# Kernel tuning notes

Hardware: AMD Instinct MI355X
Metric: run time of the kernel (lower is better)

Reference implementation:

```python
import jax, jax.numpy as jnp
import numpy as np

EMBED_DIM = 512
KERNEL = 17


def setup_inputs() -> dict:
    key = jax.random.key(0)
    ks = jax.random.split(key, 5)
    B, L, C = 2, 8192, EMBED_DIM
    s = C ** -0.5
    x = jax.random.normal(ks[0], (B, L, C), dtype=jnp.float32)
    # weights stored as (in, out); equivalent to torch Linear weight.T
    w_qkv = jax.random.normal(ks[1], (C, 3 * C), dtype=jnp.float32) * s
    w_width = jax.random.normal(ks[2], (C, 1), dtype=jnp.float32) * s
    b_width = jax.random.normal(ks[3], (1,), dtype=jnp.float32) * 0.01
    w_out = jax.random.normal(ks[4], (C, C), dtype=jnp.float32) * s
    return {"x": x, "w_qkv": w_qkv, "w_width": w_width, "b_width": b_width, "w_out": w_out}


def reference(x, w_qkv, w_width, b_width, w_out):
    B, L, C = x.shape
    K = KERNEL
    half_k = K // 2
    scale = C ** -0.5

    qkv = x @ w_qkv                      # [B,L,3C]
    q, k, v = jnp.split(qkv, 3, axis=-1)

    # learned soft window width in [1, K]
    width = jax.nn.sigmoid(x @ w_width + b_width) * (K - 1) + 1.0   # [B,L,1]

    # sliding windows of k/v: pad along L then gather K-sized windows
    k_pad = jnp.pad(k, ((0, 0), (half_k, half_k), (0, 0)))
    v_pad = jnp.pad(v, ((0, 0), (half_k, half_k), (0, 0)))
    idx = jnp.arange(L)[:, None] + jnp.arange(K)[None, :]           # [L,K]
    k_win = k_pad[:, idx]                # [B,L,K,C]
    v_win = v_pad[:, idx]                # [B,L,K,C]

    scores = jnp.einsum('blc,blkc->blk', q, k_win) * scale          # [B,L,K]

    rel_pos = jnp.abs(jnp.arange(K, dtype=jnp.float32) - half_k)    # [K]
    soft_mask = jax.nn.sigmoid((width - rel_pos) * 5.0)             # [B,L,K]
    scores = scores - (1.0 - soft_mask) * 10000.0

    attn = jax.nn.softmax(scores, axis=-1)
    out = jnp.einsum('blk,blkc->blc', attn, v_win)                  # [B,L,C]
    return (out + v) @ w_out
```

## Files before the change

kernel.cpp:

```cpp
#include <hip/hip_runtime.h>

typedef unsigned short u16;
typedef unsigned int   u32;
typedef __attribute__((ext_vector_type(8))) short          shortx8;
typedef __attribute__((ext_vector_type(8))) unsigned short ushortx8;
typedef __attribute__((ext_vector_type(4))) float          floatx4;

#define AS1 __attribute__((address_space(1)))
#define AS3 __attribute__((address_space(3)))

#define SEG 8208
#define LV  16416

__device__ __forceinline__ float b2f(u16 v) {
  return __uint_as_float(((u32)v) << 16);
}
__device__ __forceinline__ u16 f2b(float f) {
  u32 u = __float_as_uint(f);
  u += 0x7FFF + ((u >> 16) & 1);
  return (u16)(u >> 16);
}
__device__ __forceinline__ void cp16(const void* g, void* l) {
  __builtin_amdgcn_global_load_lds((AS1 u32*)g, (AS3 u32*)l, 16, 0, 0);
}

__global__ __launch_bounds__(256)
void prep(const float* __restrict__ x, const float* __restrict__ w_width,
          const float* __restrict__ b_width, const float* __restrict__ w_qkv,
          const float* __restrict__ w_out, u16* __restrict__ xb,
          float* __restrict__ width, u16* __restrict__ wqkvT,
          u16* __restrict__ woutT, u16* __restrict__ Vt) {
  __shared__ u16 tile[32][33];
  const int b = blockIdx.x;
  if (b < 4096) {
    const int lane = threadIdx.x & 63;
    const int row  = b * 4 + (threadIdx.x >> 6);
    const float* xp = x + (size_t)row * 512 + lane * 8;
    floatx4 v0 = *(const floatx4*)xp;
    floatx4 v1 = *(const floatx4*)(xp + 4);
    floatx4 w0 = *(const floatx4*)(w_width + lane * 8);
    floatx4 w1 = *(const floatx4*)(w_width + lane * 8 + 4);
    float s = 0.f;
    ushortx8 o;
#pragma unroll
    for (int j = 0; j < 4; ++j) {
      s += v0[j] * w0[j] + v1[j] * w1[j];
      o[j] = f2b(v0[j]); o[4 + j] = f2b(v1[j]);
    }
    *(ushortx8*)(xb + (size_t)row * 512 + lane * 8) = o;
#pragma unroll
    for (int m = 32; m >= 1; m >>= 1) s += __shfl_xor(s, m, 64);
    if (lane == 0)
      width[row] = 16.f / (1.f + __expf(-(s + b_width[0]))) + 1.f;
  } else if (b < 5120) {
    const float* in; u16* out; int R, C, t;
    if (b < 4864) { in = w_qkv; out = wqkvT; R = 512; C = 1536; t = b - 4096; }
    else          { in = w_out; out = woutT; R = 512; C = 512;  t = b - 4864; }
    const int nbx = C / 32;
    const int cb = (t % nbx) * 32;
    const int rb = (t / nbx) * 32;
    const int tx = threadIdx.x & 31;
    const int ty = threadIdx.x >> 5;
#pragma unroll
    for (int i = 0; i < 32; i += 8)
      tile[ty + i][tx] = f2b(in[(size_t)(rb + ty + i) * C + cb + tx]);
    __syncthreads();
#pragma unroll
    for (int i = 0; i < 32; i += 8)
      out[(size_t)(cb + ty + i) * R + rb + tx] = tile[tx][ty + i];
  } else {
    const int idx = (b - 5120) * 256 + threadIdx.x;
    const int ch = idx >> 5;
    const int k  = idx & 31;
    const int seg = k >> 4;
    const int j   = k & 15;
    const int col = seg * SEG + (j < 8 ? j : 8192 + j);
    Vt[(size_t)ch * LV + col] = 0;
  }
}

template <int MODE>
__global__ __launch_bounds__(256, 3)
void gemm_bt(const u16* __restrict__ A, const u16* __restrict__ Bt,
             void* __restrict__ C0, u16* __restrict__ Kb, u16* __restrict__ Vt) {
  const int K = 512;
  __shared__ alignas(16) u16 lds[17408];
  u16* As = lds;
  u16* Bs = lds + 8192;
  const int tid  = threadIdx.x;
  const int lane = tid & 63;
  const int wave = tid >> 6;
  const int quad = lane >> 4;
  const int lr   = lane & 15;
  const int row0 = blockIdx.x * 128;
  const int col0 = blockIdx.y * 128;
  const int wr   = (wave >> 1) * 64;
  const int wc   = (wave & 1) * 64;

  floatx4 acc[4][4];
#pragma unroll
  for (int i = 0; i < 4; ++i)
#pragma unroll
    for (int j = 0; j < 4; ++j) acc[i][j] = (floatx4)0.0f;

  int srow[4], scol[4];
#pragma unroll
  for (int p = 0; p < 4; ++p) {
    int c = p * 256 + tid;
    srow[p] = c >> 3;
    scol[p] = ((c & 7) ^ (srow[p] & 7)) * 8;
  }
  const int swz = lr & 7;

  for (int k0 = 0; k0 < K; k0 += 64) {
#pragma unroll
    for (int p = 0; p < 4; ++p)
      cp16(A + (size_t)(row0 + srow[p]) * K + k0 + scol[p], &As[(p * 256 + tid) * 8]);
#pragma unroll
    for (int p = 0; p < 4; ++p)
      cp16(Bt + (size_t)(col0 + srow[p]) * K + k0 + scol[p], &Bs[(p * 256 + tid) * 8]);
    __syncthreads();

#pragma unroll
    for (int ks = 0; ks < 2; ++ks) {
      shortx8 af[4], bf[4];
#pragma unroll
      for (int mi = 0; mi < 4; ++mi)
        af[mi] = *(const shortx8*)
            &As[((wr + mi * 16 + lr) * 8 + ((ks * 4 + quad) ^ swz)) * 8];
#pragma unroll
      for (int ni = 0; ni < 4; ++ni)
        bf[ni] = *(const shortx8*)
            &Bs[((wc + ni * 16 + lr) * 8 + ((ks * 4 + quad) ^ swz)) * 8];
#pragma unroll
      for (int mi = 0; mi < 4; ++mi)
#pragma unroll
        for (int ni = 0; ni < 4; ++ni)
          acc[mi][ni] = __builtin_amdgcn_mfma_f32_16x16x32_bf16(
              af[mi], bf[ni], acc[mi][ni], 0, 0, 0);
    }
    __syncthreads();
  }

  if constexpr (MODE == 1) {
    if (col0 < 1024) {
      u16* dst = (col0 < 512) ? (u16*)C0 : Kb;
      const int cb = col0 & 511;
#pragma unroll
      for (int mi = 0; mi < 4; ++mi)
#pragma unroll
        for (int ni = 0; ni < 4; ++ni)
#pragma unroll
          for (int r = 0; r < 4; ++r)
            lds[(wr + mi * 16 + quad * 4 + r) * 136 + wc + ni * 16 + lr] =
                f2b(acc[mi][ni][r]);
      __syncthreads();
      const int rr = tid >> 4, cc = (tid & 15) * 8;
#pragma unroll
      for (int it = 0; it < 8; ++it) {
        int row = it * 16 + rr;
        *(ushortx8*)(dst + (size_t)(row0 + row) * 512 + cb + cc) =
            *(const ushortx8*)&lds[row * 136 + cc];
      }
    } else {
      const int cb = col0 - 1024;
      const int bb = row0 >> 13, pib0 = row0 & 8191;
#pragma unroll
      for (int mi = 0; mi < 4; ++mi)
#pragma unroll
        for (int ni = 0; ni < 4; ++ni)
#pragma unroll
          for (int r = 0; r < 4; ++r)
            lds[(wc + ni * 16 + lr) * 136 + wr + mi * 16 + quad * 4 + r] =
                f2b(acc[mi][ni][r]);
      __syncthreads();
      const int rr = tid >> 4, cc = (tid & 15) * 8;
#pragma unroll
      for (int it = 0; it < 8; ++it) {
        int chl = it * 16 + rr;
        ushortx8 v = *(const ushortx8*)&lds[chl * 136 + cc];
        *(ushortx8*)(Vt + (size_t)(cb + chl) * LV + (size_t)bb * SEG + 8 + pib0 + cc) = v;
      }
    }
  } else {
    float* Cf = (float*)C0;
#pragma unroll
    for (int mi = 0; mi < 4; ++mi)
#pragma unroll
      for (int ni = 0; ni < 4; ++ni)
#pragma unroll
        for (int r = 0; r < 4; ++r) {
          int row = row0 + wr + mi * 16 + quad * 4 + r;
          int col = col0 + wc + ni * 16 + lr;
          Cf[(size_t)row * 512 + col] = acc[mi][ni][r];
        }
  }
}

__global__ __launch_bounds__(256)
void attn_mfma(const u16* __restrict__ Q, const u16* __restrict__ Kb,
               const u16* __restrict__ Vt, const float* __restrict__ width,
               u16* __restrict__ Out) {
  __shared__ float Sp[8][16][16];
  __shared__ u16   P[16][32];
  __shared__ u16   O[4][16][136];
  const int tid  = threadIdx.x;
  const int lane = tid & 63;
  const int wave = tid >> 6;
  const int quad = lane >> 4;
  const int lr   = lane & 15;
  const int p0   = blockIdx.x * 16;
  const int pib0 = p0 & 8191;
  const int bb   = p0 >> 13;

  floatx4 s0 = (floatx4)0.0f, s1 = (floatx4)0.0f;
#pragma unroll
  for (int s = 0; s < 4; ++s) {
    const int k0 = wave * 128 + s * 32 + quad * 8;
    shortx8 af = *(const shortx8*)(Q  + (size_t)(p0 + lr) * 512 + k0);
    shortx8 f0 = *(const shortx8*)(Kb + (ptrdiff_t)(p0 - 8 + lr) * 512 + k0);
    shortx8 f1 = *(const shortx8*)(Kb + (ptrdiff_t)(p0 + 8 + lr) * 512 + k0);
    s0 = __builtin_amdgcn_mfma_f32_16x16x32_bf16(af, f0, s0, 0, 0, 0);
    s1 = __builtin_amdgcn_mfma_f32_16x16x32_bf16(af, f1, s1, 0, 0, 0);
  }
#pragma unroll
  for (int r = 0; r < 4; ++r) {
    Sp[wave * 2 + 0][quad * 4 + r][lr] = s0[r];
    Sp[wave * 2 + 1][quad * 4 + r][lr] = s1[r];
  }
  __syncthreads();

  {
    const int row = tid >> 4, cg = tid & 15;
    const float scale = 0.044194173824159216f;
    const float wrow  = width[p0 + row];
    float sv[2]; float mx = -1e30f;
#pragma unroll
    for (int t = 0; t < 2; ++t) {
      const int col = t * 16 + cg;
      float s = Sp[t][row][cg] + Sp[2 + t][row][cg] +
                Sp[4 + t][row][cg] + Sp[6 + t][row][cg];
      const int d  = col - row;
      const int jb = pib0 + col - 8;
      const bool inband  = (d >= 0) && (d <= 16);
      const bool inbatch = ((unsigned)jb < 8192u);
      float rel  = fabsf((float)(d - 8));
      float mask = 1.f / (1.f + __expf(-5.f * (wrow - rel)));
      float pen  = (1.f - mask) * 10000.f;
      float val  = inband ? ((inbatch ? s * scale : 0.f) - pen) : -1e30f;
      sv[t] = val;
      mx = fmaxf(mx, val);
    }
#pragma unroll
    for (int m = 8; m >= 1; m >>= 1) mx = fmaxf(mx, __shfl_xor(mx, m, 64));
    float e0 = __expf(sv[0] - mx), e1 = __expf(sv[1] - mx);
    float sum = e0 + e1;
#pragma unroll
    for (int m = 8; m >= 1; m >>= 1) sum += __shfl_xor(sum, m, 64);
    const float inv = 1.f / sum;
    P[row][cg]      = f2b(e0 * inv + ((cg - row) == 8 ? 1.f : 0.f));
    P[row][cg + 16] = f2b(e1 * inv + ((cg + 16 - row) == 8 ? 1.f : 0.f));
  }
  __syncthreads();

  shortx8 pf = *(const shortx8*)&P[lr][quad * 8];
  const size_t cb0 = (size_t)bb * SEG + pib0;
#pragma unroll
  for (int ct = 0; ct < 8; ++ct) {
    const int ch = wave * 128 + ct * 16 + lr;
    shortx8 vf = *(const shortx8*)(Vt + (size_t)ch * LV + cb0 + quad * 8);
    floatx4 o = __builtin_amdgcn_mfma_f32_16x16x32_bf16(pf, vf, (floatx4)0.0f,
                                                        0, 0, 0);
#pragma unroll
    for (int r = 0; r < 4; ++r)
      O[wave][quad * 4 + r][ct * 16 + lr] = f2b(o[r]);
  }
  __syncthreads();
  {
    const int orow = lane >> 2;
#pragma unroll
    for (int i = 0; i < 4; ++i) {
      const int c = i * 32 + (lane & 3) * 8;
      ushortx8 v = *(const ushortx8*)&O[wave][orow][c];
      *(ushortx8*)(Out + (size_t)(p0 + orow) * 512 + wave * 128 + c) = v;
    }
  }
}

extern "C" void kernel_launch(void* const* d_in, const int* in_sizes, int n_in,
                              void* d_out, int out_size, void* d_ws, size_t ws_size,
                              hipStream_t stream) {
  const float* x       = (const float*)d_in[0];
  const float* w_qkv   = (const float*)d_in[1];
  const float* w_width = (const float*)d_in[2];
  const float* b_width = (const float*)d_in[3];
  const float* w_out   = (const float*)d_in[4];
  float* out = (float*)d_out;

  const int M = 16384, C = 512, N3 = 1536;
  char* ws = (char*)d_ws;
  u16*   xb    = (u16*)(ws);
  u16*   Qb    = (u16*)(ws + 16777216);
  u16*   Kb    = (u16*)(ws + 33554432 + 8192);
  u16*   Vt    = (u16*)(ws + 50348032);
  u16*   wqkvT = (u16*)(ws + 67158016);
  u16*   woutT = (u16*)(ws + 68730880);
  float* width = (float*)(ws + 69255168);

  dim3 blk(256);
  prep<<<dim3(5184), blk, 0, stream>>>(x, w_width, b_width, w_qkv, w_out,
                                       xb, width, wqkvT, woutT, Vt);
  gemm_bt<1><<<dim3(M / 128, N3 / 128), blk, 0, stream>>>(xb, wqkvT, Qb, Kb, Vt);
  attn_mfma<<<dim3(M / 16), blk, 0, stream>>>(Qb, Kb, Vt, width, Qb);
  gemm_bt<2><<<dim3(M / 128, C / 128), blk, 0, stream>>>(Qb, woutT, out, nullptr, nullptr);
}
```

Before: 156.9 us.

## Fuse sliding-window attention with output projection GEMM in one kernel

Merges the attention kernel and the final output-projection GEMM into a single kernel. Each block now handles 64 rows, with one wave per 16 rows computing the full 512-channel score reduction itself, so the LDS partial-sum exchange and its syncs go away. The bf16 attention output (plus v) is staged in a swizzled LDS tile and multiplied directly by woutT, which avoids writing the intermediate to global memory and a separate launch. In exchange, each block rereads woutT from global/L2, there are only 256 blocks with launch_bounds(256,1), and each thread holds large accumulator arrays, which may hurt occupancy and latency hiding.

```diff
diff --git a/kernel.cpp b/kernel.cpp
--- a/kernel.cpp
+++ b/kernel.cpp
@@ -197,94 +197,124 @@
   }
 }
 
-__global__ __launch_bounds__(256)
-void attn_mfma(const u16* __restrict__ Q, const u16* __restrict__ Kb,
-               const u16* __restrict__ Vt, const float* __restrict__ width,
-               u16* __restrict__ Out) {
-  __shared__ float Sp[8][16][16];
-  __shared__ u16   P[16][32];
-  __shared__ u16   O[4][16][136];
+__global__ __launch_bounds__(256, 1)
+void attn_fused(const u16* __restrict__ Q, const u16* __restrict__ Kb,
+                const u16* __restrict__ Vt, const float* __restrict__ width,
+                const u16* __restrict__ woutT, float* __restrict__ Out) {
+  __shared__ alignas(16) u16 Osw[64 * 256];
+  __shared__ alignas(16) u16 P[4][16][32];
   const int tid  = threadIdx.x;
   const int lane = tid & 63;
   const int wave = tid >> 6;
   const int quad = lane >> 4;
   const int lr   = lane & 15;
-  const int p0   = blockIdx.x * 16;
-  const int pib0 = p0 & 8191;
-  const int bb   = p0 >> 13;
+  const int p0   = blockIdx.x * 64;
+  const int pw   = p0 + wave * 16;
+  const int pibw = pw & 8191;
+  const int bb   = pw >> 13;
 
   floatx4 s0 = (floatx4)0.0f, s1 = (floatx4)0.0f;
-#pragma unroll
-  for (int s = 0; s < 4; ++s) {
-    const int k0 = wave * 128 + s * 32 + quad * 8;
-    shortx8 af = *(const shortx8*)(Q  + (size_t)(p0 + lr) * 512 + k0);
-    shortx8 f0 = *(const shortx8*)(Kb + (ptrdiff_t)(p0 - 8 + lr) * 512 + k0);
-    shortx8 f1 = *(const shortx8*)(Kb + (ptrdiff_t)(p0 + 8 + lr) * 512 + k0);
+#pragma unroll 4
+  for (int s = 0; s < 16; ++s) {
+    const int k0 = s * 32 + quad * 8;
+    shortx8 af = *(const shortx8*)(Q  + (size_t)(pw + lr) * 512 + k0);
+    shortx8 f0 = *(const shortx8*)(Kb + (ptrdiff_t)(pw - 8 + lr) * 512 + k0);
+    shortx8 f1 = *(const shortx8*)(Kb + (ptrdiff_t)(pw + 8 + lr) * 512 + k0);
     s0 = __builtin_amdgcn_mfma_f32_16x16x32_bf16(af, f0, s0, 0, 0, 0);
     s1 = __builtin_amdgcn_mfma_f32_16x16x32_bf16(af, f1, s1, 0, 0, 0);
   }
-#pragma unroll
-  for (int r = 0; r < 4; ++r) {
-    Sp[wave * 2 + 0][quad * 4 + r][lr] = s0[r];
-    Sp[wave * 2 + 1][quad * 4 + r][lr] = s1[r];
-  }
-  __syncthreads();
 
   {
-    const int row = tid >> 4, cg = tid & 15;
     const float scale = 0.044194173824159216f;
-    const float wrow  = width[p0 + row];
-    float sv[2]; float mx = -1e30f;
-#pragma unroll
-    for (int t = 0; t < 2; ++t) {
-      const int col = t * 16 + cg;
-      float s = Sp[t][row][cg] + Sp[2 + t][row][cg] +
-                Sp[4 + t][row][cg] + Sp[6 + t][row][cg];
-      const int d  = col - row;
-      const int jb = pib0 + col - 8;
-      const bool inband  = (d >= 0) && (d <= 16);
-      const bool inbatch = ((unsigned)jb < 8192u);
-      float rel  = fabsf((float)(d - 8));
-      float mask = 1.f / (1.f + __expf(-5.f * (wrow - rel)));
-      float pen  = (1.f - mask) * 10000.f;
-      float val  = inband ? ((inbatch ? s * scale : 0.f) - pen) : -1e30f;
-      sv[t] = val;
-      mx = fmaxf(mx, val);
-    }
-#pragma unroll
-    for (int m = 8; m >= 1; m >>= 1) mx = fmaxf(mx, __shfl_xor(mx, m, 64));
-    float e0 = __expf(sv[0] - mx), e1 = __expf(sv[1] - mx);
-    float sum = e0 + e1;
-#pragma unroll
-    for (int m = 8; m >= 1; m >>= 1) sum += __shfl_xor(sum, m, 64);
-    const float inv = 1.f / sum;
-    P[row][cg]      = f2b(e0 * inv + ((cg - row) == 8 ? 1.f : 0.f));
-    P[row][cg + 16] = f2b(e1 * inv + ((cg + 16 - row) == 8 ? 1.f : 0.f));
-  }
-  __syncthreads();
-
-  shortx8 pf = *(const shortx8*)&P[lr][quad * 8];
-  const size_t cb0 = (size_t)bb * SEG + pib0;
-#pragma unroll
-  for (int ct = 0; ct < 8; ++ct) {
-    const int ch = wave * 128 + ct * 16 + lr;
-    shortx8 vf = *(const shortx8*)(Vt + (size_t)ch * LV + cb0 + quad * 8);
-    floatx4 o = __builtin_amdgcn_mfma_f32_16x16x32_bf16(pf, vf, (floatx4)0.0f,
-                                                        0, 0, 0);
-#pragma unroll
-    for (int r = 0; r < 4; ++r)
-      O[wave][quad * 4 + r][ct * 16 + lr] = f2b(o[r]);
-  }
-  __syncthreads();
-  {
-    const int orow = lane >> 2;
-#pragma unroll
-    for (int i = 0; i < 4; ++i) {
-      const int c = i * 32 + (lane & 3) * 8;
-      ushortx8 v = *(const ushortx8*)&O[wave][orow][c];
-      *(ushortx8*)(Out + (size_t)(p0 + orow) * 512 + wave * 128 + c) = v;
-    }
-  }
+    floatx4 wv = *(const floatx4*)(width + pw + quad * 4);
+#pragma unroll
+    for (int r = 0; r < 4; ++r) {
+      const int row = quad * 4 + r;
+      const int d0  = lr - row;
+      const int d1  = d0 + 16;
+      const int jb0 = pibw + lr - 8;
+      const int jb1 = jb0 + 16;
+      float rel0 = fabsf((float)(d0 - 8));
+      float rel1 = fabsf((float)(d1 - 8));
+      float mk0 = 1.f / (1.f + __expf(-5.f * (wv[r] - rel0)));
+      float mk1 = 1.f / (1.f + __expf(-5.f * (wv[r] - rel1)));
+      float val0 = (d0 >= 0)
+          ? (((unsigned)jb0 < 8192u ? s0[r] * scale : 0.f) - (1.f - mk0) * 10000.f)
+          : -1e30f;
+      float val1 = (d1 <= 16)
+          ? (((unsigned)jb1 < 8192u ? s1[r] * scale : 0.f) - (1.f - mk1) * 10000.f)
+          : -1e30f;
+      float mx = fmaxf(val0, val1);
+#pragma unroll
+      for (int m = 8; m >= 1; m >>= 1) mx = fmaxf(mx, __shfl_xor(mx, m, 64));
+      float e0 = __expf(val0 - mx), e1 = __expf(val1 - mx);
+      float sum = e0 + e1;
+#pragma unroll
+      for (int m = 8; m >= 1; m >>= 1) sum += __shfl_xor(sum, m, 64);
+      const float inv = 1.f / sum;
+      P[wave][row][lr]      = f2b(e0 * inv + (d0 == 8 ? 1.f : 0.f));
+      P[wave][row][lr + 16] = f2b(e1 * inv + (d1 == 8 ? 1.f : 0.f));
+    }
+  }
+
+  shortx8 pf = *(const shortx8*)&P[wave][lr][quad * 8];
+  const size_t cb0 = (size_t)bb * SEG + pibw;
+  const int wc = wave * 128;
+  floatx4 acc[4][8];
+#pragma unroll
+  for (int mi = 0; mi < 4; ++mi)
+#pragma unroll
+    for (int ni = 0; ni < 8; ++ni) acc[mi][ni] = (floatx4)0.0f;
+
+#pragma unroll
+  for (int half = 0; half < 2; ++half) {
+#pragma unroll 4
+    for (int ctl = 0; ctl < 16; ++ctl) {
+      const int ch = half * 256 + ctl * 16 + lr;
+      shortx8 vf = *(const shortx8*)(Vt + (size_t)ch * LV + cb0 + quad * 8);
+      floatx4 o = __builtin_amdgcn_mfma_f32_16x16x32_bf16(pf, vf, (floatx4)0.0f,
+                                                          0, 0, 0);
+      const int c = ctl * 2 + (lr >> 3);
+#pragma unroll
+      for (int r = 0; r < 4; ++r) {
+        const int row = wave * 16 + quad * 4 + r;
+        Osw[row * 256 + (((c & ~7) | ((c & 7) ^ (row & 7))) << 3) + (lr & 7)] =
+            f2b(o[r]);
+      }
+    }
+    __syncthreads();
+
+    for (int ksl = 0; ksl < 8; ++ksl) {
+      const int kg = half * 256 + ksl * 32 + quad * 8;
+      shortx8 bfr[8], afr[4];
+#pragma unroll
+      for (int ni = 0; ni < 8; ++ni)
+        bfr[ni] = *(const shortx8*)(woutT + (size_t)(wc + ni * 16 + lr) * 512 + kg);
+#pragma unroll
+      for (int mi = 0; mi < 4; ++mi) {
+        const int row = mi * 16 + lr;
+        const int c = ksl * 4 + quad;
+        afr[mi] = *(const shortx8*)
+            &Osw[row * 256 + (((c & ~7) | ((c & 7) ^ (row & 7))) << 3)];
+      }
+#pragma unroll
+      for (int mi = 0; mi < 4; ++mi)
+#pragma unroll
+        for (int ni = 0; ni < 8; ++ni)
+          acc[mi][ni] = __builtin_amdgcn_mfma_f32_16x16x32_bf16(
+              afr[mi], bfr[ni], acc[mi][ni], 0, 0, 0);
+    }
+    if (half == 0) __syncthreads();
+  }
+
+#pragma unroll
+  for (int mi = 0; mi < 4; ++mi)
+#pragma unroll
+    for (int ni = 0; ni < 8; ++ni)
+#pragma unroll
+      for (int r = 0; r < 4; ++r)
+        Out[(size_t)(p0 + mi * 16 + quad * 4 + r) * 512 + wc + ni * 16 + lr] =
+            acc[mi][ni][r];
 }
 
 extern "C" void kernel_launch(void* const* d_in, const int* in_sizes, int n_in,
@@ -297,7 +327,7 @@
   const float* w_out   = (const float*)d_in[4];
   float* out = (float*)d_out;
 
-  const int M = 16384, C = 512, N3 = 1536;
+  const int M = 16384, N3 = 1536;
   char* ws = (char*)d_ws;
   u16*   xb    = (u16*)(ws);
   u16*   Qb    = (u16*)(ws + 16777216);
@@ -311,6 +341,5 @@
   prep<<<dim3(5184), blk, 0, stream>>>(x, w_width, b_width, w_qkv, w_out,
                                        xb, width, wqkvT, woutT, Vt);
   gemm_bt<1><<<dim3(M / 128, N3 / 128), blk, 0, stream>>>(xb, wqkvT, Qb, Kb, Vt);
-  attn_mfma<<<dim3(M / 16), blk, 0, stream>>>(Qb, Kb, Vt, width, Qb);
-  gemm_bt<2><<<dim3(M / 128, C / 128), blk, 0, stream>>>(Qb, woutT, out, nullptr, nullptr);
-}
+  attn_fused<<<dim3(M / 64), blk, 0, stream>>>(Qb, Kb, Vt, width, woutT, out);
+}
```

New measurement: 156.4 us. No clear change (-0.4%).
